# Kernel tuning notes

Measured on AMD Instinct MI355X. Metric: run time of the kernel, lower is better.

## Reference

```python
import jax, jax.numpy as jnp
import numpy as np

N = 16384      # number of PF candidates (nodes)
D_IN = 13      # pfc_input_dim
H = 16         # hidden_dim
K = 8          # kNN neighbors (includes self, dist 0, matching PyG knn(x, x, k))


def setup_inputs() -> dict:
    key = jax.random.key(0)
    ks = jax.random.split(key, 8)

    def w(k, shape):
        return (jax.random.normal(k, shape, dtype=jnp.float32) * 0.1)

    z = lambda n: jnp.zeros((n,), dtype=jnp.float32)
    return {
        "x_pfc": jax.random.normal(ks[0], (N, D_IN), dtype=jnp.float32),
        # pfc_encode: Linear(13,8) SiLU, Linear(8,16) SiLU, Linear(16,15)
        "W1": w(ks[1], (D_IN, H // 2)), "b1": z(H // 2),
        "W2": w(ks[2], (H // 2, H)),    "b2": z(H),
        "W3": w(ks[3], (H, H - 1)),     "b3": z(H - 1),
        # DynamicEdgeConv edge MLP: Linear(2H, H) SiLU
        "We": w(ks[4], (2 * H, H)),     "be": z(H),
        # ffn: Linear(H, 2H) SiLU, Linear(2H, H)
        "Wf1": w(ks[5], (H, 2 * H)),    "bf1": z(2 * H),
        "Wf2": w(ks[6], (2 * H, H)),    "bf2": z(H),
    }


def reference(x_pfc, W1, b1, W2, b2, W3, b3, We, be, Wf1, bf1, Wf2, bf2):
    silu = jax.nn.silu
    # pfc_encode (dropout = identity in eval)
    h = silu(x_pfc @ W1 + b1)
    h = silu(h @ W2 + b2)
    h = h @ W3 + b3                                   # [N, H-1]
    x = jnp.concatenate([h, x_pfc[:, -1:]], axis=1)   # [N, H]

    # Dynamic kNN graph in encoded-feature space (self included, dist 0)
    sq = jnp.sum(x * x, axis=1)                       # [N]
    d2 = sq[:, None] + sq[None, :] - 2.0 * (x @ x.T)  # [N, N] pairwise sq dist
    _, idx = jax.lax.top_k(-d2, K)                    # [N, K] neighbor indices

    # EdgeConv message: nn(cat([x_i, x_j - x_i])), mean aggregation
    x_j = x[idx]                                      # [N, K, H] gather
    x_i = x[:, None, :]                               # [N, 1, H]
    edge_in = jnp.concatenate(
        [jnp.broadcast_to(x_i, x_j.shape), x_j - x_i], axis=-1)  # [N, K, 2H]
    msg = silu(edge_in @ We + be)                     # [N, K, H]
    feats = jnp.mean(msg, axis=1)                     # [N, H]

    # ffn (dropout = identity in eval)
    f = silu(feats @ Wf1 + bf1)
    f = f @ Wf2 + bf2                                 # [N, H]
    return jnp.concatenate([f, x_pfc], axis=1)        # [N, H + D_IN]
```

## Files before the change

### kernel.cpp

```cpp
#include <hip/hip_runtime.h>
#include <math.h>

#define NPTS 16384
#define DIN 13
#define KNN 8
#define GL 12
#define BIGF 1.7014118e38f

typedef _Float16 half8 __attribute__((ext_vector_type(8)));
typedef float f32x4 __attribute__((ext_vector_type(4)));
typedef float f32x16 __attribute__((ext_vector_type(16)));

union HU4 { uint4 u; half8 h; };

__device__ __forceinline__ float silu(float v) {
    return v / (1.0f + __expf(-v));
}

#define MED3(v, a, b) __builtin_amdgcn_fmed3f((v), (a), (b))

#define INS8V(v) {                      \
    d7 = MED3((v), d6, d7);             \
    d6 = MED3((v), d5, d6);             \
    d5 = MED3((v), d4, d5);             \
    d4 = MED3((v), d3, d4);             \
    d3 = MED3((v), d2, d3);             \
    d2 = MED3((v), d1, d2);             \
    d1 = MED3((v), d0, d1);             \
    d0 = fminf((v), d0); }

#define INS12G(v) {                     \
    g11 = MED3((v), g10, g11);          \
    g10 = MED3((v), g9, g10);           \
    g9  = MED3((v), g8, g9);            \
    g8  = MED3((v), g7, g8);            \
    g7  = MED3((v), g6, g7);            \
    g6  = MED3((v), g5, g6);            \
    g5  = MED3((v), g4, g5);            \
    g4  = MED3((v), g3, g4);            \
    g3  = MED3((v), g2, g3);            \
    g2  = MED3((v), g1, g2);            \
    g1  = MED3((v), g0, g1);            \
    g0  = fminf((v), g0); }

#define CSW(p, q) { float lo_ = fminf(m##p, m##q); float hi_ = fmaxf(m##p, m##q); m##p = lo_; m##q = hi_; }

#define CLEAN16() \
    CSW(0,8) CSW(1,9) CSW(2,10) CSW(3,11) CSW(4,12) CSW(5,13) CSW(6,14) CSW(7,15) \
    CSW(0,4) CSW(1,5) CSW(2,6) CSW(3,7) CSW(8,12) CSW(9,13) CSW(10,14) CSW(11,15) \
    CSW(0,2) CSW(1,3) CSW(4,6) CSW(5,7) CSW(8,10) CSW(9,11) CSW(12,14) CSW(13,15) \
    CSW(0,1) CSW(2,3) CSW(4,5) CSW(6,7) CSW(8,9) CSW(10,11) CSW(12,13) CSW(14,15)

#define MERGE12_SHFL(mask) {                                  \
    float b0 = __shfl_xor(g0, (mask), 64);                    \
    float b1 = __shfl_xor(g1, (mask), 64);                    \
    float b2 = __shfl_xor(g2, (mask), 64);                    \
    float b3 = __shfl_xor(g3, (mask), 64);                    \
    float b4 = __shfl_xor(g4, (mask), 64);                    \
    float b5 = __shfl_xor(g5, (mask), 64);                    \
    float b6 = __shfl_xor(g6, (mask), 64);                    \
    float b7 = __shfl_xor(g7, (mask), 64);                    \
    float b8 = __shfl_xor(g8, (mask), 64);                    \
    float b9 = __shfl_xor(g9, (mask), 64);                    \
    float b10 = __shfl_xor(g10, (mask), 64);                  \
    float b11 = __shfl_xor(g11, (mask), 64);                  \
    float m0 = g0, m1 = g1, m2 = g2, m3 = g3;                 \
    float m4 = fminf(g4, b11), m5 = fminf(g5, b10);           \
    float m6 = fminf(g6, b9),  m7 = fminf(g7, b8);            \
    float m8 = fminf(g8, b7),  m9 = fminf(g9, b6);            \
    float m10 = fminf(g10, b5), m11 = fminf(g11, b4);         \
    float m12 = b3, m13 = b2, m14 = b1, m15 = b0;             \
    CLEAN16();                                                \
    g0 = m0; g1 = m1; g2 = m2; g3 = m3; g4 = m4; g5 = m5;     \
    g6 = m6; g7 = m7; g8 = m8; g9 = m9; g10 = m10; g11 = m11; }

#define MERGE12_LDS(LD) {                                     \
    float b0 = LD(0), b1 = LD(1), b2 = LD(2), b3 = LD(3);     \
    float b4 = LD(4), b5 = LD(5), b6 = LD(6), b7 = LD(7);     \
    float b8 = LD(8), b9 = LD(9), b10 = LD(10), b11 = LD(11); \
    float m0 = g0, m1 = g1, m2 = g2, m3 = g3;                 \
    float m4 = fminf(g4, b11), m5 = fminf(g5, b10);           \
    float m6 = fminf(g6, b9),  m7 = fminf(g7, b8);            \
    float m8 = fminf(g8, b7),  m9 = fminf(g9, b6);            \
    float m10 = fminf(g10, b5), m11 = fminf(g11, b4);         \
    float m12 = b3, m13 = b2, m14 = b1, m15 = b0;             \
    CLEAN16();                                                \
    g0 = m0; g1 = m1; g2 = m2; g3 = m3; g4 = m4; g5 = m5;     \
    g6 = m6; g7 = m7; g8 = m8; g9 = m9; g10 = m10; g11 = m11; }

#define MERGE8(mask) {                                   \
    float b0 = __shfl_xor(d0, (mask), 64);               \
    float b1 = __shfl_xor(d1, (mask), 64);               \
    float b2 = __shfl_xor(d2, (mask), 64);               \
    float b3 = __shfl_xor(d3, (mask), 64);               \
    float b4 = __shfl_xor(d4, (mask), 64);               \
    float b5 = __shfl_xor(d5, (mask), 64);               \
    float b6 = __shfl_xor(d6, (mask), 64);               \
    float b7 = __shfl_xor(d7, (mask), 64);               \
    float m0 = fminf(d0, b7), m1 = fminf(d1, b6);        \
    float m2 = fminf(d2, b5), m3 = fminf(d3, b4);        \
    float m4 = fminf(d4, b3), m5 = fminf(d5, b2);        \
    float m6 = fminf(d6, b1), m7 = fminf(d7, b0);        \
    CSW(0,4) CSW(1,5) CSW(2,6) CSW(3,7)                  \
    CSW(0,2) CSW(1,3) CSW(4,6) CSW(5,7)                  \
    CSW(0,1) CSW(2,3) CSW(4,5) CSW(6,7)                  \
    d0 = m0; d1 = m1; d2 = m2; d3 = m3;                  \
    d4 = m4; d5 = m5; d6 = m6; d7 = m7; }

__global__ __launch_bounds__(64) void k_encoder(
    const float* __restrict__ x_pfc,
    const float* __restrict__ W1, const float* __restrict__ b1,
    const float* __restrict__ W2, const float* __restrict__ b2,
    const float* __restrict__ W3, const float* __restrict__ b3,
    const float* __restrict__ We, const float* __restrict__ be,
    float* __restrict__ xo, _Float16* __restrict__ H, _Float16* __restrict__ L,
    _Float16* __restrict__ YH, _Float16* __restrict__ YL,
    float* __restrict__ SQF, unsigned* __restrict__ SQHL,
    float* __restrict__ ACC)
{
    __shared__ float sW1[DIN * 8];
    __shared__ float sb1[8];
    __shared__ float sW2[8 * 16];
    __shared__ float sb2[16];
    __shared__ float sW3[16 * 15];
    __shared__ float sb3[15];
    __shared__ float sWe[16 * 16];
    __shared__ float sbe[16];
    int t = threadIdx.x;
    for (int q = t; q < DIN * 8; q += 64) sW1[q] = W1[q];
    for (int q = t; q < 8; q += 64) sb1[q] = b1[q];
    for (int q = t; q < 8 * 16; q += 64) sW2[q] = W2[q];
    for (int q = t; q < 16; q += 64) sb2[q] = b2[q];
    for (int q = t; q < 16 * 15; q += 64) sW3[q] = W3[q];
    for (int q = t; q < 15; q += 64) sb3[q] = b3[q];
    for (int q = t; q < 16 * 16; q += 64) sWe[q] = We[q];
    for (int q = t; q < 16; q += 64) sbe[q] = be[q];
    __syncthreads();

    int i = blockIdx.x * 64 + t;
    float in[DIN];
#pragma unroll
    for (int d = 0; d < DIN; ++d) in[d] = x_pfc[i * DIN + d];

    float a1[8];
#pragma unroll
    for (int h = 0; h < 8; ++h) a1[h] = sb1[h];
#pragma unroll
    for (int d = 0; d < DIN; ++d) {
        float v = in[d];
#pragma unroll
        for (int h = 0; h < 8; ++h) a1[h] += v * sW1[d * 8 + h];
    }
#pragma unroll
    for (int h = 0; h < 8; ++h) a1[h] = silu(a1[h]);

    float a2[16];
#pragma unroll
    for (int h = 0; h < 16; ++h) a2[h] = sb2[h];
#pragma unroll
    for (int d = 0; d < 8; ++d) {
        float v = a1[d];
#pragma unroll
        for (int h = 0; h < 16; ++h) a2[h] += v * sW2[d * 16 + h];
    }
#pragma unroll
    for (int h = 0; h < 16; ++h) a2[h] = silu(a2[h]);

    float a3[15];
#pragma unroll
    for (int h = 0; h < 15; ++h) a3[h] = sb3[h];
#pragma unroll
    for (int d = 0; d < 16; ++d) {
        float v = a2[d];
#pragma unroll
        for (int h = 0; h < 15; ++h) a3[h] += v * sW3[d * 15 + h];
    }

    float xr[16];
#pragma unroll
    for (int h = 0; h < 15; ++h) xr[h] = a3[h];
    xr[15] = in[DIN - 1];

    float s = 0.0f;
#pragma unroll
    for (int d = 0; d < 16; ++d) s += xr[d] * xr[d];

    float accb[16];
#pragma unroll
    for (int h = 0; h < 16; ++h) accb[h] = sbe[h];
#pragma unroll
    for (int d = 0; d < 16; ++d) {
        float v = xr[d];
#pragma unroll
        for (int h = 0; h < 16; ++h) accb[h] += v * sWe[d * 16 + h];
    }

    _Float16 hb[16], lb[16], yhb[16], ylb[16];
#pragma unroll
    for (int d = 0; d < 16; ++d) {
        _Float16 h = (_Float16)xr[d];
        hb[d] = h;
        lb[d] = (_Float16)(xr[d] - (float)h);
        float y = -2.0f * xr[d];
        _Float16 yh = (_Float16)y;
        yhb[d] = yh;
        ylb[d] = (_Float16)(y - (float)yh);
    }
    {
        uint4* p;
        p = (uint4*)(H + (size_t)i * 16);  p[0] = ((uint4*)hb)[0];  p[1] = ((uint4*)hb)[1];
        p = (uint4*)(L + (size_t)i * 16);  p[0] = ((uint4*)lb)[0];  p[1] = ((uint4*)lb)[1];
        p = (uint4*)(YH + (size_t)i * 16); p[0] = ((uint4*)yhb)[0]; p[1] = ((uint4*)yhb)[1];
        p = (uint4*)(YL + (size_t)i * 16); p[0] = ((uint4*)ylb)[0]; p[1] = ((uint4*)ylb)[1];
        f32x4* xq = (f32x4*)(xo + (size_t)i * 16);
        f32x4* aq = (f32x4*)(ACC + (size_t)i * 16);
#pragma unroll
        for (int q = 0; q < 4; ++q) {
            f32x4 xv, av;
#pragma unroll
            for (int r = 0; r < 4; ++r) { xv[r] = xr[q * 4 + r]; av[r] = accb[q * 4 + r]; }
            xq[q] = xv;
            aq[q] = av;
        }
    }
    SQF[i] = s;
    {
        _Float16 sh = (_Float16)s;
        _Float16 sl = (_Float16)(s - (float)sh);
        unsigned uh = *(const unsigned short*)&sh;
        unsigned ul = *(const unsigned short*)&sl;
        SQHL[i] = (ul << 16) | uh;
    }
}

__global__ __launch_bounds__(512, 4) void k_knn(
    const _Float16* __restrict__ H, const _Float16* __restrict__ L,
    const _Float16* __restrict__ YH, const _Float16* __restrict__ YL,
    const unsigned* __restrict__ SQHL, unsigned* __restrict__ CV)
{
    __shared__ float wl[8 * GL * 32];

    int t = threadIdx.x;
    int w = t >> 6;
    int lane = t & 63;
    int r31 = lane & 31;
    int hh = lane >> 5;
    int ih = blockIdx.x >> 1;
    int jh = blockIdx.x & 1;
    int i0 = ih * 32;

    int gi = i0 + r31;
    half8 B1 = *(const half8*)(YH + (size_t)gi * 16 + hh * 8);
    half8 B2 = *(const half8*)(YL + (size_t)gi * 16 + hh * 8);
    half8 B4;
    {
        HU4 r;
        r.u.x = (hh == 0) ? 0x3C003C00u : 0u;
        r.u.y = 0u; r.u.z = 0u; r.u.w = 0u;
        B4 = r.h;
    }
    unsigned sqmask = (hh == 0) ? 0xFFFFFFFFu : 0u;

    float g0 = BIGF, g1 = BIGF, g2 = BIGF, g3 = BIGF;
    float g4 = BIGF, g5 = BIGF, g6 = BIGF, g7 = BIGF;
    float g8 = BIGF, g9 = BIGF, g10 = BIGF, g11 = BIGF;

    int jw = jh * 8192 + w * 1024;
    const _Float16* pH = H + ((size_t)(jw + r31)) * 16 + hh * 8;
    const _Float16* pL = L + ((size_t)(jw + r31)) * 16 + hh * 8;
    const unsigned* pQ = SQHL + jw + r31;
    unsigned idt0 = (unsigned)((w << 1) | hh);

#pragma unroll 4
    for (int tt = 0; tt < 32; ++tt) {
        half8 Ah = *(const half8*)(pH + (size_t)tt * 512);
        half8 Al = *(const half8*)(pL + (size_t)tt * 512);
        unsigned squ = pQ[tt * 32];
        HU4 a4;
        a4.u.x = squ & sqmask;
        a4.u.y = 0u; a4.u.z = 0u; a4.u.w = 0u;

        f32x16 c = {};
        c = __builtin_amdgcn_mfma_f32_32x32x16_f16(a4.h, B4, c, 0, 0, 0);
        c = __builtin_amdgcn_mfma_f32_32x32x16_f16(Ah, B1, c, 0, 0, 0);
        c = __builtin_amdgcn_mfma_f32_32x32x16_f16(Al, B1, c, 0, 0, 0);
        c = __builtin_amdgcn_mfma_f32_32x32x16_f16(Ah, B2, c, 0, 0, 0);

        float v0 = fminf(fminf(c[0], c[1]), c[2]);
        float v1 = fminf(fminf(c[3], c[4]), c[5]);
        float v2 = fminf(fminf(c[6], c[7]), c[8]);
        float v3 = fminf(fminf(c[9], c[10]), c[11]);
        float v4 = fminf(fminf(c[12], c[13]), c[14]);
        float v5 = fminf(fminf(v0, v1), c[15]);
        float v6 = fminf(fminf(v2, v3), v4);
        float vmin = fminf(v5, v6);

        unsigned pk = (__float_as_uint(vmin) & 0xFFFFFC00u) | (idt0 + (unsigned)(tt << 4));
        float pf = __uint_as_float(pk);
        INS12G(pf);
    }

    MERGE12_SHFL(32);

#define STORE12() if (lane < 32) {                     \
        wl[(w * GL + 0) * 32 + r31] = g0;              \
        wl[(w * GL + 1) * 32 + r31] = g1;              \
        wl[(w * GL + 2) * 32 + r31] = g2;              \
        wl[(w * GL + 3) * 32 + r31] = g3;              \
        wl[(w * GL + 4) * 32 + r31] = g4;              \
        wl[(w * GL + 5) * 32 + r31] = g5;              \
        wl[(w * GL + 6) * 32 + r31] = g6;              \
        wl[(w * GL + 7) * 32 + r31] = g7;              \
        wl[(w * GL + 8) * 32 + r31] = g8;              \
        wl[(w * GL + 9) * 32 + r31] = g9;              \
        wl[(w * GL + 10) * 32 + r31] = g10;            \
        wl[(w * GL + 11) * 32 + r31] = g11; }

    if (w >= 4) STORE12();
    __syncthreads();
    if (w < 4) {
        int pw = w + 4;
#define LD(s) wl[(pw * GL + (s)) * 32 + r31]
        MERGE12_LDS(LD);
#undef LD
    }
    __syncthreads();
    if (w == 2 || w == 3) STORE12();
    __syncthreads();
    if (w < 2) {
        int pw = w + 2;
#define LD(s) wl[(pw * GL + (s)) * 32 + r31]
        MERGE12_LDS(LD);
#undef LD
    }
    __syncthreads();
    if (w == 1) STORE12();
    __syncthreads();
    if (w == 0) {
        int pw = 1;
#define LD(s) wl[(pw * GL + (s)) * 32 + r31]
        MERGE12_LDS(LD);
#undef LD
        if (lane < 32) {
            unsigned jb = ((unsigned)jh) << 9;
            size_t base = ((size_t)jh * NPTS + (i0 + r31)) * GL;
            CV[base + 0] = __float_as_uint(g0) | jb;
            CV[base + 1] = __float_as_uint(g1) | jb;
            CV[base + 2] = __float_as_uint(g2) | jb;
            CV[base + 3] = __float_as_uint(g3) | jb;
            CV[base + 4] = __float_as_uint(g4) | jb;
            CV[base + 5] = __float_as_uint(g5) | jb;
            CV[base + 6] = __float_as_uint(g6) | jb;
            CV[base + 7] = __float_as_uint(g7) | jb;
            CV[base + 8] = __float_as_uint(g8) | jb;
            CV[base + 9] = __float_as_uint(g9) | jb;
            CV[base + 10] = __float_as_uint(g10) | jb;
            CV[base + 11] = __float_as_uint(g11) | jb;
        }
    }
#undef STORE12
}

__global__ __launch_bounds__(512, 4) void k_head(
    const float* __restrict__ x, const unsigned* __restrict__ CV,
    const float* __restrict__ SQF,
    const float* __restrict__ x_pfc, const float* __restrict__ ACC,
    const float* __restrict__ We,
    const float* __restrict__ Wf1, const float* __restrict__ bf1,
    const float* __restrict__ Wf2, const float* __restrict__ bf2,
    float* __restrict__ out)
{
    __shared__ float sWe2[16 * 16];
    __shared__ float sWf1[16 * 32];
    __shared__ float sbf1[32];
    __shared__ float sWf2[32 * 16];
    __shared__ float sbf2[16];
    __shared__ int sGrp[32][GL];
    __shared__ int cnt[32];
    __shared__ int sIdx[32 * 8];
    __shared__ float sF1[32 * 33];
    int t = threadIdx.x;
    for (int q = t; q < 16 * 16; q += 512) sWe2[q] = We[256 + q];
    for (int q = t; q < 16 * 32; q += 512) sWf1[q] = Wf1[q];
    for (int q = t; q < 32; q += 512) sbf1[q] = bf1[q];
    for (int q = t; q < 32 * 16; q += 512) sWf2[q] = Wf2[q];
    for (int q = t; q < 16; q += 512) sbf2[q] = bf2[q];

    int i0 = blockIdx.x * 32;

    if (t < 64) {
        int pi = t & 31;
        int hf = t >> 5;
        const f32x4* c = (const f32x4*)(CV + ((size_t)hf * NPTS + (i0 + pi)) * GL);
        f32x4 c0 = c[0], c1 = c[1], c2 = c[2];
        float g0 = c0[0], g1 = c0[1], g2 = c0[2], g3 = c0[3];
        float g4 = c1[0], g5 = c1[1], g6 = c1[2], g7 = c1[3];
        float g8 = c2[0], g9 = c2[1], g10 = c2[2], g11 = c2[3];
        MERGE12_SHFL(32);
        if (t < 32) {
            cnt[pi] = 0;
#define DECJB(gk, s) { unsigned id_ = __float_as_uint(gk) & 0x3FFu;          \
            sGrp[pi][s] = (int)(((id_ >> 9) & 1) * 8192 + ((id_ >> 1) & 7) * 1024 + \
                                ((id_ >> 4) & 31) * 32 + (id_ & 1) * 4); }
            DECJB(g0, 0) DECJB(g1, 1) DECJB(g2, 2) DECJB(g3, 3)
            DECJB(g4, 4) DECJB(g5, 5) DECJB(g6, 6) DECJB(g7, 7)
            DECJB(g8, 8) DECJB(g9, 9) DECJB(g10, 10) DECJB(g11, 11)
#undef DECJB
        }
    }
    __syncthreads();

    int l = t & 15;
    int pt = t >> 4;
    int ql = l & 3;
    int qd = l >> 2;
    int i = i0 + pt;

    float xi[16];
    {
        const f32x4* xiv = (const f32x4*)(x + (size_t)i * 16);
#pragma unroll
        for (int q = 0; q < 4; ++q) {
            f32x4 a = xiv[q];
#pragma unroll
            for (int r = 0; r < 4; ++r) xi[q * 4 + r] = a[r];
        }
    }
    f32x4 xiq = ((const f32x4*)(x + (size_t)i * 16))[ql];

    float val[12];
    float d0 = BIGF, d1 = BIGF, d2 = BIGF, d3 = BIGF;
    float d4 = BIGF, d5 = BIGF, d6 = BIGF, d7 = BIGF;
#pragma unroll
    for (int g = 0; g < GL; ++g) {
        int jb = sGrp[pt][g];
        float vg = BIGF;
#pragma unroll
        for (int rho = 0; rho < 4; ++rho) {
            f32x4 a = *((const f32x4*)(x + ((size_t)(jb + rho * 8)) * 16) + l);
            float qdot = xiq[0] * a[0];
            qdot = fmaf(xiq[1], a[1], qdot);
            qdot = fmaf(xiq[2], a[2], qdot);
            qdot = fmaf(xiq[3], a[3], qdot);
            qdot += __shfl_xor(qdot, 1, 64);
            qdot += __shfl_xor(qdot, 2, 64);
            float v = fmaf(qdot, -2.0f, SQF[jb + rho * 8 + qd]);
            vg = (ql == rho) ? v : vg;
        }
        val[g] = vg;
        INS8V(vg);
    }

    MERGE8(1);
    MERGE8(2);
    MERGE8(4);
    MERGE8(8);
    float kth = d7;

#pragma unroll
    for (int g = 0; g < GL; ++g) {
        float v = val[g];
        if (v <= kth) {
            int j = sGrp[pt][g] + ql * 8 + qd;
            int p = atomicAdd(&cnt[pt], 1);
            if (p < KNN) sIdx[pt * 8 + p] = j;
        }
    }
    __syncthreads();

    int e8 = l & 7;
    int j = sIdx[pt * 8 + e8];

    float xd[16];
    {
        const f32x4* xjv = (const f32x4*)(x + (size_t)j * 16);
#pragma unroll
        for (int q = 0; q < 4; ++q) {
            f32x4 a = xjv[q];
#pragma unroll
            for (int r = 0; r < 4; ++r) xd[q * 4 + r] = a[r] - xi[q * 4 + r];
        }
    }

    float acc[16];
    {
        const f32x4* av = (const f32x4*)(ACC + (size_t)i * 16);
#pragma unroll
        for (int q = 0; q < 4; ++q) {
            f32x4 a = av[q];
#pragma unroll
            for (int r = 0; r < 4; ++r) acc[q * 4 + r] = a[r];
        }
    }
#pragma unroll
    for (int d = 0; d < 16; ++d) {
        float v = xd[d];
#pragma unroll
        for (int h = 0; h < 16; ++h) acc[h] += v * sWe2[d * 16 + h];
    }

    float feats[16];
#pragma unroll
    for (int h = 0; h < 16; ++h) feats[h] = silu(acc[h]);

#pragma unroll
    for (int mask = 1; mask <= 4; mask <<= 1) {
#pragma unroll
        for (int h = 0; h < 16; ++h) feats[h] += __shfl_xor(feats[h], mask, 64);
    }
#pragma unroll
    for (int h = 0; h < 16; ++h) feats[h] *= 0.125f;

    float p0 = sbf1[l];
    float p1 = sbf1[l + 16];
#pragma unroll
    for (int k = 0; k < 16; ++k) {
        float v = feats[k];
        p0 = fmaf(v, sWf1[k * 32 + l], p0);
        p1 = fmaf(v, sWf1[k * 32 + l + 16], p1);
    }
    p0 = silu(p0);
    p1 = silu(p1);
    sF1[pt * 33 + l] = p0;
    sF1[pt * 33 + 16 + l] = p1;
    __syncthreads();

    float o = sbf2[l];
#pragma unroll
    for (int k = 0; k < 32; ++k)
        o = fmaf(sF1[pt * 33 + k], sWf2[k * 16 + l], o);

    out[(size_t)i * 29 + l] = o;
    if (l < DIN) out[(size_t)i * 29 + 16 + l] = x_pfc[i * DIN + l];
}

extern "C" void kernel_launch(void* const* d_in, const int* in_sizes, int n_in,
                              void* d_out, int out_size, void* d_ws, size_t ws_size,
                              hipStream_t stream)
{
    const float* x_pfc = (const float*)d_in[0];
    const float* W1 = (const float*)d_in[1];
    const float* b1 = (const float*)d_in[2];
    const float* W2 = (const float*)d_in[3];
    const float* b2 = (const float*)d_in[4];
    const float* W3 = (const float*)d_in[5];
    const float* b3 = (const float*)d_in[6];
    const float* We = (const float*)d_in[7];
    const float* be = (const float*)d_in[8];
    const float* Wf1 = (const float*)d_in[9];
    const float* bf1 = (const float*)d_in[10];
    const float* Wf2 = (const float*)d_in[11];
    const float* bf2 = (const float*)d_in[12];
    float* out = (float*)d_out;

    float* xw = (float*)d_ws;
    float* ACCa = xw + (size_t)NPTS * 16;
    _Float16* Ha = (_Float16*)(ACCa + (size_t)NPTS * 16);
    _Float16* La = Ha + (size_t)NPTS * 16;
    _Float16* YHa = La + (size_t)NPTS * 16;
    _Float16* YLa = YHa + (size_t)NPTS * 16;
    float* SQFa = (float*)(YLa + (size_t)NPTS * 16);
    unsigned* SQHLa = (unsigned*)(SQFa + NPTS);
    unsigned* CVa = SQHLa + NPTS;

    hipLaunchKernelGGL(k_encoder, dim3(NPTS / 64), dim3(64), 0, stream,
                       x_pfc, W1, b1, W2, b2, W3, b3, We, be,
                       xw, Ha, La, YHa, YLa, SQFa, SQHLa, ACCa);
    hipLaunchKernelGGL(k_knn, dim3(NPTS / 32 * 2), dim3(512), 0, stream,
                       Ha, La, YHa, YLa, SQHLa, CVa);
    hipLaunchKernelGGL(k_head, dim3(NPTS / 32), dim3(512), 0, stream,
                       xw, CVa, SQFa, x_pfc, ACCa, We, Wf1, bf1, Wf2, bf2, out);
}
```

Measured before the change: 152.7 us.

## Fuse kNN search and head kernels, preload squared norms into LDS accumulator

Merges the kNN candidate-search kernel and the head kernel into one kernel, so the per-block candidate list stays in shared memory and the global CV round trip and one launch go away. Each block now covers all 16384 columns with 8 waves of 64 tiles, where before two blocks per row group each covered half. The squared-norm term, previously a fourth MFMA fed from packed fp16 hi/lo values, is now loaded as fp32 from a 64 KB LDS copy straight into the MFMA accumulator. The 64 KB LDS union cuts occupancy and halves the grid to 512 blocks, which may leave the GPU less well filled.

```diff
diff --git a/kernel.cpp b/kernel.cpp
--- a/kernel.cpp
+++ b/kernel.cpp
@@ -11,7 +11,7 @@
 typedef float f32x4 __attribute__((ext_vector_type(4)));
 typedef float f32x16 __attribute__((ext_vector_type(16)));
 
-union HU4 { uint4 u; half8 h; };
+union C16 { f32x16 w; f32x4 q[4]; };
 
 __device__ __forceinline__ float silu(float v) {
     return v / (1.0f + __expf(-v));
@@ -115,8 +115,7 @@
     const float* __restrict__ We, const float* __restrict__ be,
     float* __restrict__ xo, _Float16* __restrict__ H, _Float16* __restrict__ L,
     _Float16* __restrict__ YH, _Float16* __restrict__ YL,
-    float* __restrict__ SQF, unsigned* __restrict__ SQHL,
-    float* __restrict__ ACC)
+    float* __restrict__ SQF, float* __restrict__ ACC)
 {
     __shared__ float sW1[DIN * 8];
     __shared__ float sb1[8];
@@ -224,314 +223,283 @@
         }
     }
     SQF[i] = s;
-    {
-        _Float16 sh = (_Float16)s;
-        _Float16 sl = (_Float16)(s - (float)sh);
-        unsigned uh = *(const unsigned short*)&sh;
-        unsigned ul = *(const unsigned short*)&sl;
-        SQHL[i] = (ul << 16) | uh;
-    }
 }
 
-__global__ __launch_bounds__(512, 4) void k_knn(
+__global__ __launch_bounds__(512, 4) void k_knn_head(
     const _Float16* __restrict__ H, const _Float16* __restrict__ L,
     const _Float16* __restrict__ YH, const _Float16* __restrict__ YL,
-    const unsigned* __restrict__ SQHL, unsigned* __restrict__ CV)
-{
-    __shared__ float wl[8 * GL * 32];
-
-    int t = threadIdx.x;
-    int w = t >> 6;
-    int lane = t & 63;
-    int r31 = lane & 31;
-    int hh = lane >> 5;
-    int ih = blockIdx.x >> 1;
-    int jh = blockIdx.x & 1;
-    int i0 = ih * 32;
-
-    int gi = i0 + r31;
-    half8 B1 = *(const half8*)(YH + (size_t)gi * 16 + hh * 8);
-    half8 B2 = *(const half8*)(YL + (size_t)gi * 16 + hh * 8);
-    half8 B4;
-    {
-        HU4 r;
-        r.u.x = (hh == 0) ? 0x3C003C00u : 0u;
-        r.u.y = 0u; r.u.z = 0u; r.u.w = 0u;
-        B4 = r.h;
-    }
-    unsigned sqmask = (hh == 0) ? 0xFFFFFFFFu : 0u;
-
-    float g0 = BIGF, g1 = BIGF, g2 = BIGF, g3 = BIGF;
-    float g4 = BIGF, g5 = BIGF, g6 = BIGF, g7 = BIGF;
-    float g8 = BIGF, g9 = BIGF, g10 = BIGF, g11 = BIGF;
-
-    int jw = jh * 8192 + w * 1024;
-    const _Float16* pH = H + ((size_t)(jw + r31)) * 16 + hh * 8;
-    const _Float16* pL = L + ((size_t)(jw + r31)) * 16 + hh * 8;
-    const unsigned* pQ = SQHL + jw + r31;
-    unsigned idt0 = (unsigned)((w << 1) | hh);
-
-#pragma unroll 4
-    for (int tt = 0; tt < 32; ++tt) {
-        half8 Ah = *(const half8*)(pH + (size_t)tt * 512);
-        half8 Al = *(const half8*)(pL + (size_t)tt * 512);
-        unsigned squ = pQ[tt * 32];
-        HU4 a4;
-        a4.u.x = squ & sqmask;
-        a4.u.y = 0u; a4.u.z = 0u; a4.u.w = 0u;
-
-        f32x16 c = {};
-        c = __builtin_amdgcn_mfma_f32_32x32x16_f16(a4.h, B4, c, 0, 0, 0);
-        c = __builtin_amdgcn_mfma_f32_32x32x16_f16(Ah, B1, c, 0, 0, 0);
-        c = __builtin_amdgcn_mfma_f32_32x32x16_f16(Al, B1, c, 0, 0, 0);
-        c = __builtin_amdgcn_mfma_f32_32x32x16_f16(Ah, B2, c, 0, 0, 0);
-
-        float v0 = fminf(fminf(c[0], c[1]), c[2]);
-        float v1 = fminf(fminf(c[3], c[4]), c[5]);
-        float v2 = fminf(fminf(c[6], c[7]), c[8]);
-        float v3 = fminf(fminf(c[9], c[10]), c[11]);
-        float v4 = fminf(fminf(c[12], c[13]), c[14]);
-        float v5 = fminf(fminf(v0, v1), c[15]);
-        float v6 = fminf(fminf(v2, v3), v4);
-        float vmin = fminf(v5, v6);
-
-        unsigned pk = (__float_as_uint(vmin) & 0xFFFFFC00u) | (idt0 + (unsigned)(tt << 4));
-        float pf = __uint_as_float(pk);
-        INS12G(pf);
-    }
-
-    MERGE12_SHFL(32);
-
-#define STORE12() if (lane < 32) {                     \
-        wl[(w * GL + 0) * 32 + r31] = g0;              \
-        wl[(w * GL + 1) * 32 + r31] = g1;              \
-        wl[(w * GL + 2) * 32 + r31] = g2;              \
-        wl[(w * GL + 3) * 32 + r31] = g3;              \
-        wl[(w * GL + 4) * 32 + r31] = g4;              \
-        wl[(w * GL + 5) * 32 + r31] = g5;              \
-        wl[(w * GL + 6) * 32 + r31] = g6;              \
-        wl[(w * GL + 7) * 32 + r31] = g7;              \
-        wl[(w * GL + 8) * 32 + r31] = g8;              \
-        wl[(w * GL + 9) * 32 + r31] = g9;              \
-        wl[(w * GL + 10) * 32 + r31] = g10;            \
-        wl[(w * GL + 11) * 32 + r31] = g11; }
-
-    if (w >= 4) STORE12();
-    __syncthreads();
-    if (w < 4) {
-        int pw = w + 4;
-#define LD(s) wl[(pw * GL + (s)) * 32 + r31]
-        MERGE12_LDS(LD);
-#undef LD
-    }
-    __syncthreads();
-    if (w == 2 || w == 3) STORE12();
-    __syncthreads();
-    if (w < 2) {
-        int pw = w + 2;
-#define LD(s) wl[(pw * GL + (s)) * 32 + r31]
-        MERGE12_LDS(LD);
-#undef LD
-    }
-    __syncthreads();
-    if (w == 1) STORE12();
-    __syncthreads();
-    if (w == 0) {
-        int pw = 1;
-#define LD(s) wl[(pw * GL + (s)) * 32 + r31]
-        MERGE12_LDS(LD);
-#undef LD
-        if (lane < 32) {
-            unsigned jb = ((unsigned)jh) << 9;
-            size_t base = ((size_t)jh * NPTS + (i0 + r31)) * GL;
-            CV[base + 0] = __float_as_uint(g0) | jb;
-            CV[base + 1] = __float_as_uint(g1) | jb;
-            CV[base + 2] = __float_as_uint(g2) | jb;
-            CV[base + 3] = __float_as_uint(g3) | jb;
-            CV[base + 4] = __float_as_uint(g4) | jb;
-            CV[base + 5] = __float_as_uint(g5) | jb;
-            CV[base + 6] = __float_as_uint(g6) | jb;
-            CV[base + 7] = __float_as_uint(g7) | jb;
-            CV[base + 8] = __float_as_uint(g8) | jb;
-            CV[base + 9] = __float_as_uint(g9) | jb;
-            CV[base + 10] = __float_as_uint(g10) | jb;
-            CV[base + 11] = __float_as_uint(g11) | jb;
-        }
-    }
-#undef STORE12
-}
-
-__global__ __launch_bounds__(512, 4) void k_head(
-    const float* __restrict__ x, const unsigned* __restrict__ CV,
-    const float* __restrict__ SQF,
+    const float* __restrict__ SQF, const float* __restrict__ x,
     const float* __restrict__ x_pfc, const float* __restrict__ ACC,
     const float* __restrict__ We,
     const float* __restrict__ Wf1, const float* __restrict__ bf1,
     const float* __restrict__ Wf2, const float* __restrict__ bf2,
     float* __restrict__ out)
 {
-    __shared__ float sWe2[16 * 16];
-    __shared__ float sWf1[16 * 32];
-    __shared__ float sbf1[32];
-    __shared__ float sWf2[32 * 16];
-    __shared__ float sbf2[16];
-    __shared__ int sGrp[32][GL];
-    __shared__ int cnt[32];
-    __shared__ int sIdx[32 * 8];
-    __shared__ float sF1[32 * 33];
+    __shared__ union SU {
+        float knn[16384];
+        struct {
+            float we2[256]; float wf1[512]; float bf1s[32];
+            float wf2[512]; float bf2s[16];
+            int cnt[32]; int idx[256];
+            float f1[32 * 33];
+        } h;
+    } S;
+    __shared__ unsigned sList[32 * GL];
+
     int t = threadIdx.x;
-    for (int q = t; q < 16 * 16; q += 512) sWe2[q] = We[256 + q];
-    for (int q = t; q < 16 * 32; q += 512) sWf1[q] = Wf1[q];
-    for (int q = t; q < 32; q += 512) sbf1[q] = bf1[q];
-    for (int q = t; q < 32 * 16; q += 512) sWf2[q] = Wf2[q];
-    for (int q = t; q < 16; q += 512) sbf2[q] = bf2[q];
-
+    int w = t >> 6;
+    int lane = t & 63;
+    int r31 = lane & 31;
+    int hh = lane >> 5;
     int i0 = blockIdx.x * 32;
 
-    if (t < 64) {
-        int pi = t & 31;
-        int hf = t >> 5;
-        const f32x4* c = (const f32x4*)(CV + ((size_t)hf * NPTS + (i0 + pi)) * GL);
-        f32x4 c0 = c[0], c1 = c[1], c2 = c[2];
-        float g0 = c0[0], g1 = c0[1], g2 = c0[2], g3 = c0[3];
-        float g4 = c1[0], g5 = c1[1], g6 = c1[2], g7 = c1[3];
-        float g8 = c2[0], g9 = c2[1], g10 = c2[2], g11 = c2[3];
+    {
+        int gi = i0 + r31;
+        half8 B1 = *(const half8*)(YH + (size_t)gi * 16 + hh * 8);
+        half8 B2 = *(const half8*)(YL + (size_t)gi * 16 + hh * 8);
+
+        {
+            const f32x4* src = (const f32x4*)SQF;
+            f32x4* dst = (f32x4*)S.knn;
+            for (int q = t; q < 4096; q += 512) dst[q] = src[q];
+        }
+
+        float g0 = BIGF, g1 = BIGF, g2 = BIGF, g3 = BIGF;
+        float g4 = BIGF, g5 = BIGF, g6 = BIGF, g7 = BIGF;
+        float g8 = BIGF, g9 = BIGF, g10 = BIGF, g11 = BIGF;
+
+        const _Float16* pH = H + ((size_t)(w * 2048 + r31)) * 16 + hh * 8;
+        const _Float16* pL = L + ((size_t)(w * 2048 + r31)) * 16 + hh * 8;
+        const float* sqb = S.knn + w * 2048 + hh * 4;
+        unsigned idt = (unsigned)((w << 1) | hh);
+
+        __syncthreads();
+
+#pragma unroll 2
+        for (int tt = 0; tt < 64; ++tt) {
+            half8 Ah = *(const half8*)(pH + (size_t)tt * 512);
+            half8 Al = *(const half8*)(pL + (size_t)tt * 512);
+            const f32x4* s_ = (const f32x4*)(sqb + tt * 32);
+
+            C16 c;
+            c.q[0] = s_[0]; c.q[1] = s_[2]; c.q[2] = s_[4]; c.q[3] = s_[6];
+            c.w = __builtin_amdgcn_mfma_f32_32x32x16_f16(Ah, B1, c.w, 0, 0, 0);
+            c.w = __builtin_amdgcn_mfma_f32_32x32x16_f16(Al, B1, c.w, 0, 0, 0);
+            c.w = __builtin_amdgcn_mfma_f32_32x32x16_f16(Ah, B2, c.w, 0, 0, 0);
+
+            float v0 = fminf(fminf(c.w[0], c.w[1]), c.w[2]);
+            float v1 = fminf(fminf(c.w[3], c.w[4]), c.w[5]);
+            float v2 = fminf(fminf(c.w[6], c.w[7]), c.w[8]);
+            float v3 = fminf(fminf(c.w[9], c.w[10]), c.w[11]);
+            float v4 = fminf(fminf(c.w[12], c.w[13]), c.w[14]);
+            float v5 = fminf(fminf(v0, v1), c.w[15]);
+            float v6 = fminf(fminf(v2, v3), v4);
+            float vmin = fminf(v5, v6);
+
+            unsigned pk = (__float_as_uint(vmin) & 0xFFFFFC00u)
+                        | (idt + (unsigned)(tt << 4));
+            float pf = __uint_as_float(pk);
+            INS12G(pf);
+        }
+
         MERGE12_SHFL(32);
-        if (t < 32) {
-            cnt[pi] = 0;
-#define DECJB(gk, s) { unsigned id_ = __float_as_uint(gk) & 0x3FFu;          \
-            sGrp[pi][s] = (int)(((id_ >> 9) & 1) * 8192 + ((id_ >> 1) & 7) * 1024 + \
-                                ((id_ >> 4) & 31) * 32 + (id_ & 1) * 4); }
-            DECJB(g0, 0) DECJB(g1, 1) DECJB(g2, 2) DECJB(g3, 3)
-            DECJB(g4, 4) DECJB(g5, 5) DECJB(g6, 6) DECJB(g7, 7)
-            DECJB(g8, 8) DECJB(g9, 9) DECJB(g10, 10) DECJB(g11, 11)
-#undef DECJB
-        }
-    }
+
+        __syncthreads();
+
+#define STORE12() if (lane < 32) {                           \
+            S.knn[(w * GL + 0) * 32 + r31] = g0;             \
+            S.knn[(w * GL + 1) * 32 + r31] = g1;             \
+            S.knn[(w * GL + 2) * 32 + r31] = g2;             \
+            S.knn[(w * GL + 3) * 32 + r31] = g3;             \
+            S.knn[(w * GL + 4) * 32 + r31] = g4;             \
+            S.knn[(w * GL + 5) * 32 + r31] = g5;             \
+            S.knn[(w * GL + 6) * 32 + r31] = g6;             \
+            S.knn[(w * GL + 7) * 32 + r31] = g7;             \
+            S.knn[(w * GL + 8) * 32 + r31] = g8;             \
+            S.knn[(w * GL + 9) * 32 + r31] = g9;             \
+            S.knn[(w * GL + 10) * 32 + r31] = g10;           \
+            S.knn[(w * GL + 11) * 32 + r31] = g11; }
+
+        if (w >= 4) STORE12();
+        __syncthreads();
+        if (w < 4) {
+            int pw = w + 4;
+#define LD(s) S.knn[(pw * GL + (s)) * 32 + r31]
+            MERGE12_LDS(LD);
+#undef LD
+        }
+        __syncthreads();
+        if (w == 2 || w == 3) STORE12();
+        __syncthreads();
+        if (w < 2) {
+            int pw = w + 2;
+#define LD(s) S.knn[(pw * GL + (s)) * 32 + r31]
+            MERGE12_LDS(LD);
+#undef LD
+        }
+        __syncthreads();
+        if (w == 1) STORE12();
+        __syncthreads();
+        if (w == 0) {
+            int pw = 1;
+#define LD(s) S.knn[(pw * GL + (s)) * 32 + r31]
+            MERGE12_LDS(LD);
+#undef LD
+            if (lane < 32) {
+                sList[r31 * GL + 0] = __float_as_uint(g0);
+                sList[r31 * GL + 1] = __float_as_uint(g1);
+                sList[r31 * GL + 2] = __float_as_uint(g2);
+                sList[r31 * GL + 3] = __float_as_uint(g3);
+                sList[r31 * GL + 4] = __float_as_uint(g4);
+                sList[r31 * GL + 5] = __float_as_uint(g5);
+                sList[r31 * GL + 6] = __float_as_uint(g6);
+                sList[r31 * GL + 7] = __float_as_uint(g7);
+                sList[r31 * GL + 8] = __float_as_uint(g8);
+                sList[r31 * GL + 9] = __float_as_uint(g9);
+                sList[r31 * GL + 10] = __float_as_uint(g10);
+                sList[r31 * GL + 11] = __float_as_uint(g11);
+            }
+        }
+#undef STORE12
+    }
+
     __syncthreads();
 
-    int l = t & 15;
-    int pt = t >> 4;
-    int ql = l & 3;
-    int qd = l >> 2;
-    int i = i0 + pt;
-
-    float xi[16];
     {
-        const f32x4* xiv = (const f32x4*)(x + (size_t)i * 16);
-#pragma unroll
-        for (int q = 0; q < 4; ++q) {
-            f32x4 a = xiv[q];
-#pragma unroll
-            for (int r = 0; r < 4; ++r) xi[q * 4 + r] = a[r];
-        }
-    }
-    f32x4 xiq = ((const f32x4*)(x + (size_t)i * 16))[ql];
-
-    float val[12];
-    float d0 = BIGF, d1 = BIGF, d2 = BIGF, d3 = BIGF;
-    float d4 = BIGF, d5 = BIGF, d6 = BIGF, d7 = BIGF;
-#pragma unroll
-    for (int g = 0; g < GL; ++g) {
-        int jb = sGrp[pt][g];
-        float vg = BIGF;
-#pragma unroll
-        for (int rho = 0; rho < 4; ++rho) {
-            f32x4 a = *((const f32x4*)(x + ((size_t)(jb + rho * 8)) * 16) + l);
-            float qdot = xiq[0] * a[0];
-            qdot = fmaf(xiq[1], a[1], qdot);
-            qdot = fmaf(xiq[2], a[2], qdot);
-            qdot = fmaf(xiq[3], a[3], qdot);
-            qdot += __shfl_xor(qdot, 1, 64);
-            qdot += __shfl_xor(qdot, 2, 64);
-            float v = fmaf(qdot, -2.0f, SQF[jb + rho * 8 + qd]);
-            vg = (ql == rho) ? v : vg;
-        }
-        val[g] = vg;
-        INS8V(vg);
-    }
-
-    MERGE8(1);
-    MERGE8(2);
-    MERGE8(4);
-    MERGE8(8);
-    float kth = d7;
-
-#pragma unroll
-    for (int g = 0; g < GL; ++g) {
-        float v = val[g];
-        if (v <= kth) {
-            int j = sGrp[pt][g] + ql * 8 + qd;
-            int p = atomicAdd(&cnt[pt], 1);
-            if (p < KNN) sIdx[pt * 8 + p] = j;
-        }
-    }
-    __syncthreads();
-
-    int e8 = l & 7;
-    int j = sIdx[pt * 8 + e8];
-
-    float xd[16];
-    {
-        const f32x4* xjv = (const f32x4*)(x + (size_t)j * 16);
-#pragma unroll
-        for (int q = 0; q < 4; ++q) {
-            f32x4 a = xjv[q];
-#pragma unroll
-            for (int r = 0; r < 4; ++r) xd[q * 4 + r] = a[r] - xi[q * 4 + r];
-        }
-    }
-
-    float acc[16];
-    {
-        const f32x4* av = (const f32x4*)(ACC + (size_t)i * 16);
-#pragma unroll
-        for (int q = 0; q < 4; ++q) {
-            f32x4 a = av[q];
-#pragma unroll
-            for (int r = 0; r < 4; ++r) acc[q * 4 + r] = a[r];
-        }
-    }
-#pragma unroll
-    for (int d = 0; d < 16; ++d) {
-        float v = xd[d];
-#pragma unroll
-        for (int h = 0; h < 16; ++h) acc[h] += v * sWe2[d * 16 + h];
-    }
-
-    float feats[16];
-#pragma unroll
-    for (int h = 0; h < 16; ++h) feats[h] = silu(acc[h]);
-
-#pragma unroll
-    for (int mask = 1; mask <= 4; mask <<= 1) {
-#pragma unroll
-        for (int h = 0; h < 16; ++h) feats[h] += __shfl_xor(feats[h], mask, 64);
-    }
-#pragma unroll
-    for (int h = 0; h < 16; ++h) feats[h] *= 0.125f;
-
-    float p0 = sbf1[l];
-    float p1 = sbf1[l + 16];
-#pragma unroll
-    for (int k = 0; k < 16; ++k) {
-        float v = feats[k];
-        p0 = fmaf(v, sWf1[k * 32 + l], p0);
-        p1 = fmaf(v, sWf1[k * 32 + l + 16], p1);
-    }
-    p0 = silu(p0);
-    p1 = silu(p1);
-    sF1[pt * 33 + l] = p0;
-    sF1[pt * 33 + 16 + l] = p1;
-    __syncthreads();
-
-    float o = sbf2[l];
-#pragma unroll
-    for (int k = 0; k < 32; ++k)
-        o = fmaf(sF1[pt * 33 + k], sWf2[k * 16 + l], o);
-
-    out[(size_t)i * 29 + l] = o;
-    if (l < DIN) out[(size_t)i * 29 + 16 + l] = x_pfc[i * DIN + l];
+        for (int q = t; q < 16 * 16; q += 512) S.h.we2[q] = We[256 + q];
+        for (int q = t; q < 16 * 32; q += 512) S.h.wf1[q] = Wf1[q];
+        for (int q = t; q < 32; q += 512) S.h.bf1s[q] = bf1[q];
+        for (int q = t; q < 32 * 16; q += 512) S.h.wf2[q] = Wf2[q];
+        for (int q = t; q < 16; q += 512) S.h.bf2s[q] = bf2[q];
+        if (t < 32) S.h.cnt[t] = 0;
+        __syncthreads();
+
+        int l = t & 15;
+        int pt = t >> 4;
+        int ql = l & 3;
+        int qd = l >> 2;
+        int i = i0 + pt;
+
+        float xi[16];
+        {
+            const f32x4* xiv = (const f32x4*)(x + (size_t)i * 16);
+#pragma unroll
+            for (int q = 0; q < 4; ++q) {
+                f32x4 a = xiv[q];
+#pragma unroll
+                for (int r = 0; r < 4; ++r) xi[q * 4 + r] = a[r];
+            }
+        }
+        f32x4 xiq = ((const f32x4*)(x + (size_t)i * 16))[ql];
+
+        float val[12];
+        int jbs[12];
+        float d0 = BIGF, d1 = BIGF, d2 = BIGF, d3 = BIGF;
+        float d4 = BIGF, d5 = BIGF, d6 = BIGF, d7 = BIGF;
+#pragma unroll
+        for (int g = 0; g < GL; ++g) {
+            unsigned id = sList[pt * GL + g] & 0x3FFu;
+            int jb = (int)(((id >> 1) & 7) * 2048 + (id >> 4) * 32 + (id & 1) * 4);
+            jbs[g] = jb;
+            float vg = BIGF;
+#pragma unroll
+            for (int rho = 0; rho < 4; ++rho) {
+                f32x4 a = *((const f32x4*)(x + ((size_t)(jb + rho * 8)) * 16) + l);
+                float qdot = xiq[0] * a[0];
+                qdot = fmaf(xiq[1], a[1], qdot);
+                qdot = fmaf(xiq[2], a[2], qdot);
+                qdot = fmaf(xiq[3], a[3], qdot);
+                qdot += __shfl_xor(qdot, 1, 64);
+                qdot += __shfl_xor(qdot, 2, 64);
+                float v = fmaf(qdot, -2.0f, SQF[jb + rho * 8 + qd]);
+                vg = (ql == rho) ? v : vg;
+            }
+            val[g] = vg;
+            INS8V(vg);
+        }
+
+        MERGE8(1);
+        MERGE8(2);
+        MERGE8(4);
+        MERGE8(8);
+        float kth = d7;
+
+#pragma unroll
+        for (int g = 0; g < GL; ++g) {
+            float v = val[g];
+            if (v <= kth) {
+                int j = jbs[g] + ql * 8 + qd;
+                int p = atomicAdd(&S.h.cnt[pt], 1);
+                if (p < KNN) S.h.idx[pt * 8 + p] = j;
+            }
+        }
+        __syncthreads();
+
+        int e8 = l & 7;
+        int j = S.h.idx[pt * 8 + e8];
+
+        float xd[16];
+        {
+            const f32x4* xjv = (const f32x4*)(x + (size_t)j * 16);
+#pragma unroll
+            for (int q = 0; q < 4; ++q) {
+                f32x4 a = xjv[q];
+#pragma unroll
+                for (int r = 0; r < 4; ++r) xd[q * 4 + r] = a[r] - xi[q * 4 + r];
+            }
+        }
+
+        float acc[16];
+        {
+            const f32x4* av = (const f32x4*)(ACC + (size_t)i * 16);
+#pragma unroll
+            for (int q = 0; q < 4; ++q) {
+                f32x4 a = av[q];
+#pragma unroll
+                for (int r = 0; r < 4; ++r) acc[q * 4 + r] = a[r];
+            }
+        }
+#pragma unroll
+        for (int d = 0; d < 16; ++d) {
+            float v = xd[d];
+#pragma unroll
+            for (int h = 0; h < 16; ++h) acc[h] += v * S.h.we2[d * 16 + h];
+        }
+
+        float feats[16];
+#pragma unroll
+        for (int h = 0; h < 16; ++h) feats[h] = silu(acc[h]);
+
+#pragma unroll
+        for (int mask = 1; mask <= 4; mask <<= 1) {
+#pragma unroll
+            for (int h = 0; h < 16; ++h) feats[h] += __shfl_xor(feats[h], mask, 64);
+        }
+#pragma unroll
+        for (int h = 0; h < 16; ++h) feats[h] *= 0.125f;
+
+        float p0 = S.h.bf1s[l];
+        float p1 = S.h.bf1s[l + 16];
+#pragma unroll
+        for (int k = 0; k < 16; ++k) {
+            float v = feats[k];
+            p0 = fmaf(v, S.h.wf1[k * 32 + l], p0);
+            p1 = fmaf(v, S.h.wf1[k * 32 + l + 16], p1);
+        }
+        p0 = silu(p0);
+        p1 = silu(p1);
+        S.h.f1[pt * 33 + l] = p0;
+        S.h.f1[pt * 33 + 16 + l] = p1;
+        __syncthreads();
+
+        float o = S.h.bf2s[l];
+#pragma unroll
+        for (int k = 0; k < 32; ++k)
+            o = fmaf(S.h.f1[pt * 33 + k], S.h.wf2[k * 16 + l], o);
+
+        out[(size_t)i * 29 + l] = o;
+        if (l < DIN) out[(size_t)i * 29 + 16 + l] = x_pfc[i * DIN + l];
+    }
 }
 
 extern "C" void kernel_launch(void* const* d_in, const int* in_sizes, int n_in,
@@ -560,14 +528,11 @@
     _Float16* YHa = La + (size_t)NPTS * 16;
     _Float16* YLa = YHa + (size_t)NPTS * 16;
     float* SQFa = (float*)(YLa + (size_t)NPTS * 16);
-    unsigned* SQHLa = (unsigned*)(SQFa + NPTS);
-    unsigned* CVa = SQHLa + NPTS;
 
     hipLaunchKernelGGL(k_encoder, dim3(NPTS / 64), dim3(64), 0, stream,
                        x_pfc, W1, b1, W2, b2, W3, b3, We, be,
-                       xw, Ha, La, YHa, YLa, SQFa, SQHLa, ACCa);
-    hipLaunchKernelGGL(k_knn, dim3(NPTS / 32 * 2), dim3(512), 0, stream,
-                       Ha, La, YHa, YLa, SQHLa, CVa);
-    hipLaunchKernelGGL(k_head, dim3(NPTS / 32), dim3(512), 0, stream,
-                       xw, CVa, SQFa, x_pfc, ACCa, We, Wf1, bf1, Wf2, bf2, out);
+                       xw, Ha, La, YHa, YLa, SQFa, ACCa);
+    hipLaunchKernelGGL(k_knn_head, dim3(NPTS / 32), dim3(512), 0, stream,
+                       Ha, La, YHa, YLa, SQFa, xw, x_pfc, ACCa,
+                       We, Wf1, bf1, Wf2, bf2, out);
 }
```

Measured after the change: 137.0 us. 1.12x faster.
